# Performance work log

Measured on AMD Instinct MI355X. Metric: run time of the kernel, lower is better.

Reference implementation:

```python
import jax, jax.numpy as jnp
import numpy as np

N = 50000
E = 800000


def _degrees(src, dst):
    ones = jnp.ones((E,), dtype=jnp.float32)
    indeg = jax.ops.segment_sum(ones, dst, num_segments=N)
    outdeg = jax.ops.segment_sum(ones, src, num_segments=N)
    return indeg, outdeg


def _aggregate(h, src, dst):
    # update_all(copy_src, sum): gather src features, scatter-add to dst
    return jax.ops.segment_sum(h[src], dst, num_segments=N)


def _graph_conv(h, src, dst, innorm, outnorm, W, b):
    h = h * outnorm[:, None]
    h = _aggregate(h, src, dst)
    h = h * innorm[:, None]
    return h @ W + b


def setup_inputs() -> dict:
    key = jax.random.key(0)
    ks = jax.random.split(key, 8)
    d_in, d_hid, d_out = 128, 128, 64
    inp = {
        "features": jax.random.normal(ks[0], (N, d_in), dtype=jnp.float32),
        "src": jax.random.randint(ks[1], (E,), 0, N, dtype=jnp.int32),
        "dst": jax.random.randint(ks[2], (E,), 0, N, dtype=jnp.int32),
        "W0": jax.random.normal(ks[3], (d_in, d_hid), dtype=jnp.float32) / np.sqrt(d_in),
        "b0": jnp.zeros((d_hid,), dtype=jnp.float32),
        "W1": jax.random.normal(ks[4], (d_hid, d_hid), dtype=jnp.float32) / np.sqrt(d_hid),
        "b1": jnp.zeros((d_hid,), dtype=jnp.float32),
        "W2": jax.random.normal(ks[5], (d_hid, d_hid), dtype=jnp.float32) / np.sqrt(d_hid),
        "b2": jnp.zeros((d_hid,), dtype=jnp.float32),
        "W3": jax.random.normal(ks[6], (d_hid, d_out), dtype=jnp.float32) / np.sqrt(d_hid),
        "b3": jnp.zeros((d_out,), dtype=jnp.float32),
    }
    return inp


def reference(features, src, dst, W0, b0, W1, b1, W2, b2, W3, b3):
    indeg, outdeg = _degrees(src, dst)
    innorm = jnp.power(jnp.clip(indeg, 1.0, None), -0.5)
    outnorm = jnp.power(jnp.clip(outdeg, 1.0, None), -0.5)

    # input GraphConv + relu
    h = jax.nn.relu(_graph_conv(features, src, dst, innorm, outnorm, W0, b0))

    # GResConv blocks: graph_res=True, raw_res=True, dropout=0 (identity)
    for (W, b) in ((W1, b1), (W2, b2)):
        res = features * innorm[:, None]          # pre-norm (in-degree)
        res = _aggregate(res, src, dst)
        res = res * innorm[:, None]               # post-norm (in-degree)
        h = jax.nn.relu(_graph_conv(h, src, dst, innorm, outnorm, W, b) + res)

    # output GraphConv (no activation)
    return _graph_conv(h, src, dst, innorm, outnorm, W3, b3)
```

## Files before the change

kernel.cpp:

```cpp
#include <hip/hip_runtime.h>


#define GN 50000
#define GE 800000
#define SCAN_CHUNK 1024
#define DEG_BLOCKS 64
#define DEG_SLICE 12500
#define HALF_NODES 25000
#define HALF_WORDS 12500

__device__ __forceinline__ float u2f(unsigned int u) { return __uint_as_float(u); }

__device__ __forceinline__ unsigned int bfpack(float a, float b) {
  unsigned int ua = __float_as_uint(a); ua = (ua + 0x7fffu + ((ua >> 16) & 1u)) >> 16;
  unsigned int ub = __float_as_uint(b); ub = (ub + 0x7fffu + ((ub >> 16) & 1u)) >> 16;
  return ua | (ub << 16);
}

__device__ __forceinline__ void bfunpack8(uint4 u, float* f) {
  f[0] = u2f(u.x << 16); f[1] = u2f(u.x & 0xffff0000u);
  f[2] = u2f(u.y << 16); f[3] = u2f(u.y & 0xffff0000u);
  f[4] = u2f(u.z << 16); f[5] = u2f(u.z & 0xffff0000u);
  f[6] = u2f(u.w << 16); f[7] = u2f(u.w & 0xffff0000u);
}

__global__ __launch_bounds__(256) void degrees_lds_kernel(
    const int* __restrict__ src, const int* __restrict__ dst,
    unsigned int* __restrict__ partials, int E) {
  __shared__ unsigned int hist[HALF_WORDS];
  for (int i = threadIdx.x; i < HALF_WORDS; i += 256) hist[i] = 0u;
  __syncthreads();
  int b    = blockIdx.x & 63;
  int half = (blockIdx.x >> 6) & 1;
  int dir  = blockIdx.x >> 7;
  const int* __restrict__ idx = dir ? src : dst;
  int lo = half * HALF_NODES, hi = lo + HALF_NODES;
  int s = b * DEG_SLICE;
  int e = min(s + DEG_SLICE, E);
  for (int i = s + threadIdx.x; i < e; i += 256) {
    int node = idx[i];
    if (node >= lo && node < hi) {
      int local = node - lo;
      atomicAdd(&hist[local >> 1], 1u << ((local & 1) << 4));
    }
  }
  __syncthreads();
  unsigned int* outp = partials + (((size_t)dir * 2 + half) * DEG_BLOCKS + b) * HALF_WORDS;
  for (int i = threadIdx.x; i < HALF_WORDS; i += 256) outp[i] = hist[i];
}

__global__ void degrees_reduce_kernel(const unsigned int* __restrict__ partials,
                                      int* __restrict__ indeg, float* __restrict__ innorm,
                                      float* __restrict__ outnorm,
                                      unsigned int* __restrict__ rel16pk) {
  int g = blockIdx.x * blockDim.x + threadIdx.x;
  if (g >= 2 * HALF_WORDS) return;
  int half = (g >= HALF_WORDS) ? 1 : 0;
  int w = g - half * HALF_WORDS;
  int n0 = half * HALF_NODES + 2 * w;
  unsigned int inLo = 0, inHi = 0, outLo = 0, outHi = 0;
  const unsigned int* pIn  = partials + ((size_t)(0 * 2 + half) * DEG_BLOCKS) * HALF_WORDS + w;
  const unsigned int* pOut = partials + ((size_t)(1 * 2 + half) * DEG_BLOCKS) * HALF_WORDS + w;
#pragma unroll 4
  for (int b = 0; b < DEG_BLOCKS; b++) {
    rel16pk[((size_t)b * GN + n0) >> 1] = inLo | (inHi << 16);
    unsigned int v = pIn[(size_t)b * HALF_WORDS];
    inLo += v & 0xffffu; inHi += v >> 16;
    unsigned int u = pOut[(size_t)b * HALF_WORDS];
    outLo += u & 0xffffu; outHi += u >> 16;
  }
  indeg[n0]     = (int)inLo;
  indeg[n0 + 1] = (int)inHi;
  innorm[n0]      = rsqrtf((float)max((int)inLo, 1));
  innorm[n0 + 1]  = rsqrtf((float)max((int)inHi, 1));
  outnorm[n0]     = rsqrtf((float)max((int)outLo, 1));
  outnorm[n0 + 1] = rsqrtf((float)max((int)outHi, 1));
}

__global__ __launch_bounds__(256) void scan_blocksums(const int* __restrict__ deg,
                                                      int* __restrict__ bsums, int n) {
  int tid = threadIdx.x;
  int i = blockIdx.x * SCAN_CHUNK + tid * 4;
  int s = 0;
  if (i + 3 < n) {
    int4 v = *(const int4*)(deg + i);
    s = v.x + v.y + v.z + v.w;
  } else {
    for (int j = 0; j < 4; j++) if (i + j < n) s += deg[i + j];
  }
  for (int off = 32; off; off >>= 1) s += __shfl_down(s, off);
  __shared__ int ws[4];
  if ((tid & 63) == 0) ws[tid >> 6] = s;
  __syncthreads();
  if (tid == 0) bsums[blockIdx.x] = ws[0] + ws[1] + ws[2] + ws[3];
}

__global__ void scan_bsums(const int* __restrict__ bsums, int* __restrict__ bpref,
                           int nb, int* __restrict__ offsets, int n) {
  int tid = threadIdx.x;
  int v = (tid < nb) ? bsums[tid] : 0;
  int incl = v;
  for (int off = 1; off < 64; off <<= 1) {
    int t = __shfl_up(incl, off);
    if (tid >= off) incl += t;
  }
  if (tid < nb) bpref[tid] = incl - v;
  if (tid == 63) offsets[n] = incl;
}

__global__ __launch_bounds__(256) void scan_final(const int* __restrict__ deg,
                                                  const int* __restrict__ bpref,
                                                  int* __restrict__ offsets, int n) {
  int tid = threadIdx.x;
  int i = blockIdx.x * SCAN_CHUNK + tid * 4;
  int v[4];
#pragma unroll
  for (int j = 0; j < 4; j++) v[j] = (i + j < n) ? deg[i + j] : 0;
  int tsum = v[0] + v[1] + v[2] + v[3];
  int incl = tsum;
  for (int off = 1; off < 64; off <<= 1) {
    int t = __shfl_up(incl, off);
    if ((tid & 63) >= off) incl += t;
  }
  __shared__ int wsum[4];
  int wid = tid >> 6, lane = tid & 63;
  if (lane == 63) wsum[wid] = incl;
  __syncthreads();
  int wpref = 0;
  for (int w = 0; w < wid; w++) wpref += wsum[w];
  int run = bpref[blockIdx.x] + wpref + incl - tsum;
#pragma unroll
  for (int j = 0; j < 4; j++) {
    if (i + j < n) offsets[i + j] = run;
    run += v[j];
  }
}

__global__ __launch_bounds__(256) void fill_csr_lds_kernel(
    const int* __restrict__ src, const int* __restrict__ dst,
    const int* __restrict__ offsets, const unsigned short* __restrict__ rel16,
    int* __restrict__ csr, int E) {
  __shared__ unsigned int cnt[HALF_WORDS];
  for (int i = threadIdx.x; i < HALF_WORDS; i += 256) cnt[i] = 0u;
  __syncthreads();
  int b    = blockIdx.x & 63;
  int half = blockIdx.x >> 6;
  int lo = half * HALF_NODES, hi = lo + HALF_NODES;
  int s = b * DEG_SLICE;
  int e = min(s + DEG_SLICE, E);
  const unsigned short* relb = rel16 + (size_t)b * GN;
  for (int i = s + threadIdx.x; i < e; i += 256) {
    int d = dst[i];
    if (d >= lo && d < hi) {
      int local = d - lo;
      int sh = (local & 1) << 4;
      unsigned int old = atomicAdd(&cnt[local >> 1], 1u << sh);
      int rank = (int)((old >> sh) & 0xffffu);
      int pos = offsets[d] + (int)relb[d] + rank;
      csr[pos] = src[i];
    }
  }
}

__global__ __launch_bounds__(256) void f32_to_bf16_kernel(const float* __restrict__ in,
                                                          uint4* __restrict__ out, int n8) {
  int t = blockIdx.x * blockDim.x + threadIdx.x;
  if (t >= n8) return;
  const float4* in4 = (const float4*)in;
  float4 f0 = in4[2 * t], f1 = in4[2 * t + 1];
  uint4 o;
  o.x = bfpack(f0.x, f0.y); o.y = bfpack(f0.z, f0.w);
  o.z = bfpack(f1.x, f1.y); o.w = bfpack(f1.z, f1.w);
  out[t] = o;
}

__global__ __launch_bounds__(256) void aggregate128_bf16_kernel(
    const uint4* __restrict__ hq, const float* __restrict__ gscale,
    const float* __restrict__ wscale, const int* __restrict__ offsets,
    const int* __restrict__ csr, float* __restrict__ out, int n) {
  int node = blockIdx.x * 4 + (threadIdx.x >> 6);
  if (node >= n) return;
  int lane = threadIdx.x & 63;
  int c = lane & 15;
  int p = lane >> 4;
  int s = offsets[node], e = offsets[node + 1];
  float acc[8];
#pragma unroll
  for (int j = 0; j < 8; j++) acc[j] = 0.f;
  int i = s + p;
  for (; i + 4 < e; i += 8) {
    int sn0 = csr[i], sn1 = csr[i + 4];
    uint4 u0 = hq[(size_t)sn0 * 16 + c];
    uint4 u1 = hq[(size_t)sn1 * 16 + c];
    float s0 = gscale[sn0], s1 = gscale[sn1];
    float f0[8], f1[8];
    bfunpack8(u0, f0); bfunpack8(u1, f1);
#pragma unroll
    for (int j = 0; j < 8; j++) acc[j] += f0[j] * s0 + f1[j] * s1;
  }
  if (i < e) {
    int sn = csr[i];
    uint4 u = hq[(size_t)sn * 16 + c];
    float sc = gscale[sn];
    float f[8];
    bfunpack8(u, f);
#pragma unroll
    for (int j = 0; j < 8; j++) acc[j] += f[j] * sc;
  }
#pragma unroll
  for (int off = 32; off >= 16; off >>= 1)
#pragma unroll
    for (int j = 0; j < 8; j++) acc[j] += __shfl_down(acc[j], off);
  if (lane < 16) {
    float w = wscale[node];
    float4* orow = (float4*)(out + (size_t)node * 128);
    orow[2 * c]     = make_float4(acc[0] * w, acc[1] * w, acc[2] * w, acc[3] * w);
    orow[2 * c + 1] = make_float4(acc[4] * w, acc[5] * w, acc[6] * w, acc[7] * w);
  }
}

__global__ __launch_bounds__(256) void aggregate_dual_bf16_kernel(
    const uint4* __restrict__ hq, const float* __restrict__ g1,
    const float* __restrict__ g2, const float* __restrict__ wscale,
    const int* __restrict__ offsets, const int* __restrict__ csr,
    float* __restrict__ out1, float* __restrict__ out2, int n) {
  int node = blockIdx.x * 4 + (threadIdx.x >> 6);
  if (node >= n) return;
  int lane = threadIdx.x & 63;
  int c = lane & 15;
  int p = lane >> 4;
  int s = offsets[node], e = offsets[node + 1];
  float a1[8], a2[8];
#pragma unroll
  for (int j = 0; j < 8; j++) { a1[j] = 0.f; a2[j] = 0.f; }
  int i = s + p;
  for (; i + 4 < e; i += 8) {
    int sn0 = csr[i], sn1 = csr[i + 4];
    uint4 u0 = hq[(size_t)sn0 * 16 + c];
    uint4 u1 = hq[(size_t)sn1 * 16 + c];
    float g1a = g1[sn0], g2a = g2[sn0];
    float g1b = g1[sn1], g2b = g2[sn1];
    float f0[8], f1[8];
    bfunpack8(u0, f0); bfunpack8(u1, f1);
#pragma unroll
    for (int j = 0; j < 8; j++) {
      a1[j] += f0[j] * g1a + f1[j] * g1b;
      a2[j] += f0[j] * g2a + f1[j] * g2b;
    }
  }
  if (i < e) {
    int sn = csr[i];
    uint4 u = hq[(size_t)sn * 16 + c];
    float g1a = g1[sn], g2a = g2[sn];
    float f[8];
    bfunpack8(u, f);
#pragma unroll
    for (int j = 0; j < 8; j++) { a1[j] += f[j] * g1a; a2[j] += f[j] * g2a; }
  }
#pragma unroll
  for (int off = 32; off >= 16; off >>= 1)
#pragma unroll
    for (int j = 0; j < 8; j++) {
      a1[j] += __shfl_down(a1[j], off);
      a2[j] += __shfl_down(a2[j], off);
    }
  if (lane < 16) {
    float w = wscale[node];
    float4* o1 = (float4*)(out1 + (size_t)node * 128);
    float4* o2 = (float4*)(out2 + (size_t)node * 128);
    o1[2 * c]     = make_float4(a1[0] * w, a1[1] * w, a1[2] * w, a1[3] * w);
    o1[2 * c + 1] = make_float4(a1[4] * w, a1[5] * w, a1[6] * w, a1[7] * w);
    o2[2 * c]     = make_float4(a2[0] * w, a2[1] * w, a2[2] * w, a2[3] * w);
    o2[2 * c + 1] = make_float4(a2[4] * w, a2[5] * w, a2[6] * w, a2[7] * w);
  }
}

__global__ __launch_bounds__(256) void aggregate64_bf16_kernel(
    const uint4* __restrict__ hq, const float* __restrict__ gscale,
    const float* __restrict__ wscale, const float* __restrict__ bias,
    const int* __restrict__ offsets, const int* __restrict__ csr,
    float* __restrict__ out, int n) {
  int node = blockIdx.x * 4 + (threadIdx.x >> 6);
  if (node >= n) return;
  int lane = threadIdx.x & 63;
  int c = lane & 7;
  int p = lane >> 3;
  int s = offsets[node], e = offsets[node + 1];
  float acc[8];
#pragma unroll
  for (int j = 0; j < 8; j++) acc[j] = 0.f;
  int i = s + p;
  for (; i + 8 < e; i += 16) {
    int sn0 = csr[i], sn1 = csr[i + 8];
    uint4 u0 = hq[(size_t)sn0 * 8 + c];
    uint4 u1 = hq[(size_t)sn1 * 8 + c];
    float s0 = gscale[sn0], s1 = gscale[sn1];
    float f0[8], f1[8];
    bfunpack8(u0, f0); bfunpack8(u1, f1);
#pragma unroll
    for (int j = 0; j < 8; j++) acc[j] += f0[j] * s0 + f1[j] * s1;
  }
  if (i < e) {
    int sn = csr[i];
    uint4 u = hq[(size_t)sn * 8 + c];
    float sc = gscale[sn];
    float f[8];
    bfunpack8(u, f);
#pragma unroll
    for (int j = 0; j < 8; j++) acc[j] += f[j] * sc;
  }
#pragma unroll
  for (int off = 32; off >= 8; off >>= 1)
#pragma unroll
    for (int j = 0; j < 8; j++) acc[j] += __shfl_down(acc[j], off);
  if (lane < 8) {
    float w = wscale[node];
    const float4* bp = (const float4*)bias;
    float4 b0 = bp[2 * c], b1 = bp[2 * c + 1];
    float4* orow = (float4*)(out + (size_t)node * 64);
    orow[2 * c]     = make_float4(acc[0] * w + b0.x, acc[1] * w + b0.y,
                                  acc[2] * w + b0.z, acc[3] * w + b0.w);
    orow[2 * c + 1] = make_float4(acc[4] * w + b1.x, acc[5] * w + b1.y,
                                  acc[6] * w + b1.z, acc[7] * w + b1.w);
  }
}

template <int DOUT, bool RELU, bool HAS_BIAS, bool ADD_RES, bool OUT_BF16>
__global__ __launch_bounds__(256) void gemm_kernel(
    const float* __restrict__ A, const float* __restrict__ W,
    const float* __restrict__ bias, const float* __restrict__ res,
    void* __restrict__ outv, int n) {
  __shared__ float Wl[128 * DOUT];
  __shared__ float Al[32 * 128];
  for (int i = threadIdx.x; i < 128 * DOUT / 4; i += 256)
    ((float4*)Wl)[i] = ((const float4*)W)[i];
  int row0 = blockIdx.x * 32;
  for (int i = threadIdx.x; i < 32 * 32; i += 256) {
    int r = i >> 5, cc = i & 31;
    int gr = row0 + r;
    float4 v = make_float4(0.f, 0.f, 0.f, 0.f);
    if (gr < n) v = *((const float4*)(A + (size_t)gr * 128) + cc);
    *((float4*)(Al + r * 128) + cc) = v;
  }
  __syncthreads();
  constexpr int CG = DOUT / 4;
  constexpr int RG = 256 / CG;
  constexpr int RPT = 32 / RG;
  int tc = threadIdx.x % CG;
  int tr = threadIdx.x / CG;
  float4 acc[RPT];
#pragma unroll
  for (int r = 0; r < RPT; r++) acc[r] = make_float4(0.f, 0.f, 0.f, 0.f);
  for (int k0 = 0; k0 < 128; k0 += 4) {
    float4 av[RPT];
#pragma unroll
    for (int r = 0; r < RPT; r++)
      av[r] = *((const float4*)(Al + (tr * RPT + r) * 128 + k0));
#pragma unroll
    for (int kk = 0; kk < 4; kk++) {
      float4 w = *((const float4*)(Wl + (k0 + kk) * DOUT) + tc);
#pragma unroll
      for (int r = 0; r < RPT; r++) {
        float a = (&av[r].x)[kk];
        acc[r].x += a * w.x; acc[r].y += a * w.y;
        acc[r].z += a * w.z; acc[r].w += a * w.w;
      }
    }
  }
  float4 b = make_float4(0.f, 0.f, 0.f, 0.f);
  if (HAS_BIAS) b = ((const float4*)bias)[tc];
#pragma unroll
  for (int r = 0; r < RPT; r++) {
    int gr = row0 + tr * RPT + r;
    if (gr < n) {
      float4 o = acc[r];
      o.x += b.x; o.y += b.y; o.z += b.z; o.w += b.w;
      if (ADD_RES) {
        float4 rr = *((const float4*)(res + (size_t)gr * DOUT) + tc);
        o.x += rr.x; o.y += rr.y; o.z += rr.z; o.w += rr.w;
      }
      if (RELU) {
        o.x = fmaxf(o.x, 0.f); o.y = fmaxf(o.y, 0.f);
        o.z = fmaxf(o.z, 0.f); o.w = fmaxf(o.w, 0.f);
      }
      if (OUT_BF16) {
        uint2 pk;
        pk.x = bfpack(o.x, o.y); pk.y = bfpack(o.z, o.w);
        unsigned int* up = (unsigned int*)outv;
        *(uint2*)(up + (size_t)gr * (DOUT / 2) + tc * 2) = pk;
      } else {
        float* outp = (float*)outv;
        *((float4*)(outp + (size_t)gr * DOUT) + tc) = o;
      }
    }
  }
}

extern "C" void kernel_launch(void* const* d_in, const int* in_sizes, int n_in,
                              void* d_out, int out_size, void* d_ws, size_t ws_size,
                              hipStream_t stream) {
  const float* features = (const float*)d_in[0];
  const int*   src      = (const int*)d_in[1];
  const int*   dst      = (const int*)d_in[2];
  const float* W0 = (const float*)d_in[3];
  const float* b0 = (const float*)d_in[4];
  const float* W1 = (const float*)d_in[5];
  const float* b1 = (const float*)d_in[6];
  const float* W2 = (const float*)d_in[7];
  const float* b2 = (const float*)d_in[8];
  const float* W3 = (const float*)d_in[9];
  const float* b3 = (const float*)d_in[10];
  float* out = (float*)d_out;
  const int N = GN, E = GE;

  char* ws = (char*)d_ws;
  size_t off = 0;
  auto alloc = [&](size_t bytes) -> void* {
    void* p = ws + off;
    off = (off + bytes + 255) & ~(size_t)255;
    return p;
  };
  unsigned int* partials = (unsigned int*)alloc((size_t)2 * 2 * DEG_BLOCKS * HALF_WORDS * 4);
  unsigned int* rel16pk  = (unsigned int*)alloc((size_t)DEG_BLOCKS * GN * 2);
  int*   indeg   = (int*)alloc((size_t)N * 4);
  float* innorm  = (float*)alloc((size_t)N * 4);
  float* outnorm = (float*)alloc((size_t)N * 4);
  int*   offsets = (int*)alloc((size_t)(N + 1) * 4);
  int*   csr     = (int*)alloc((size_t)E * 4);
  int*   bsums   = (int*)alloc((size_t)256 * 4);
  int*   bpref   = (int*)alloc((size_t)256 * 4);
  float* res     = (float*)alloc((size_t)N * 128 * 4);
  float* bufA    = (float*)alloc((size_t)N * 128 * 4);
  float* bufB    = (float*)alloc((size_t)N * 128 * 4);
  uint4* hbf     = (uint4*)alloc((size_t)N * 128 * 2);
  (void)ws_size; (void)in_sizes; (void)n_in; (void)out_size;

  uint4* fbf = (uint4*)bufB;
  uint4* Ybf = (uint4*)res;

  degrees_lds_kernel<<<256, 256, 0, stream>>>(src, dst, partials, E);
  degrees_reduce_kernel<<<(2 * HALF_WORDS + 255) / 256, 256, 0, stream>>>(
      partials, indeg, innorm, outnorm, rel16pk);

  int nb = (N + SCAN_CHUNK - 1) / SCAN_CHUNK;
  scan_blocksums<<<nb, 256, 0, stream>>>(indeg, bsums, N);
  scan_bsums<<<1, 64, 0, stream>>>(bsums, bpref, nb, offsets, N);
  scan_final<<<nb, 256, 0, stream>>>(indeg, bpref, offsets, N);

  fill_csr_lds_kernel<<<128, 256, 0, stream>>>(
      src, dst, offsets, (const unsigned short*)rel16pk, csr, E);

  f32_to_bf16_kernel<<<(N * 128 / 8 + 255) / 256, 256, 0, stream>>>(
      features, fbf, N * 128 / 8);

  int aggGrid  = (N + 3) / 4;
  int gemmGrid = (N + 31) / 32;

  aggregate_dual_bf16_kernel<<<aggGrid, 256, 0, stream>>>(
      fbf, outnorm, innorm, innorm, offsets, csr, bufA, res, N);
  gemm_kernel<128, true, true, false, true><<<gemmGrid, 256, 0, stream>>>(
      bufA, W0, b0, nullptr, hbf, N);
  aggregate128_bf16_kernel<<<aggGrid, 256, 0, stream>>>(
      hbf, outnorm, innorm, offsets, csr, bufA, N);
  gemm_kernel<128, true, true, true, true><<<gemmGrid, 256, 0, stream>>>(
      bufA, W1, b1, res, hbf, N);
  aggregate128_bf16_kernel<<<aggGrid, 256, 0, stream>>>(
      hbf, outnorm, innorm, offsets, csr, bufA, N);
  gemm_kernel<128, true, true, true, false><<<gemmGrid, 256, 0, stream>>>(
      bufA, W2, b2, res, bufB, N);
  gemm_kernel<64, false, false, false, true><<<gemmGrid, 256, 0, stream>>>(
      bufB, W3, nullptr, nullptr, Ybf, N);
  aggregate64_bf16_kernel<<<aggGrid, 256, 0, stream>>>(
      Ybf, outnorm, innorm, b3, offsets, csr, out, N);
}
```

Before: 428.5 us.

## Replace FP32 LDS GEMMs with bf16 MFMA GEMMs using split-precision weights

Replaces the scalar FP32 shared-memory GEMM with an MFMA 16x16x32 bf16 kernel. Weights are pre-split into high and low bf16 parts so the weight side keeps near-FP32 accuracy, and activations are fed as bf16. The aggregation kernels now write bf16 outputs directly, which halves their write traffic and the GEMM read traffic. In exchange the activations lose precision before each matmul, and the GEMM epilogue does scalar 2-byte stores with uncoalesced residual reads.

```diff
diff --git a/kernel.cpp b/kernel.cpp
--- a/kernel.cpp
+++ b/kernel.cpp
@@ -9,14 +9,18 @@
 #define HALF_NODES 25000
 #define HALF_WORDS 12500
 
+typedef __attribute__((ext_vector_type(8))) short bf16x8;
+typedef __attribute__((ext_vector_type(4))) float f32x4;
+
 __device__ __forceinline__ float u2f(unsigned int u) { return __uint_as_float(u); }
 
+__device__ __forceinline__ unsigned int bfr(float a) {
+  unsigned int u = __float_as_uint(a);
+  return (u + 0x7fffu + ((u >> 16) & 1u)) >> 16;
+}
 __device__ __forceinline__ unsigned int bfpack(float a, float b) {
-  unsigned int ua = __float_as_uint(a); ua = (ua + 0x7fffu + ((ua >> 16) & 1u)) >> 16;
-  unsigned int ub = __float_as_uint(b); ub = (ub + 0x7fffu + ((ub >> 16) & 1u)) >> 16;
-  return ua | (ub << 16);
-}
-
+  return bfr(a) | (bfr(b) << 16);
+}
 __device__ __forceinline__ void bfunpack8(uint4 u, float* f) {
   f[0] = u2f(u.x << 16); f[1] = u2f(u.x & 0xffff0000u);
   f[2] = u2f(u.y << 16); f[3] = u2f(u.y & 0xffff0000u);
@@ -174,10 +178,31 @@
   out[t] = o;
 }
 
+__global__ __launch_bounds__(256) void wconvert_kernel(
+    const float* __restrict__ W0, const float* __restrict__ W1,
+    const float* __restrict__ W2, const float* __restrict__ W3,
+    unsigned short* __restrict__ wt) {
+  int e = blockIdx.x * 256 + threadIdx.x;
+  if (e >= 3 * 16384 + 8192) return;
+  int m, local, N;
+  if (e < 49152) { m = e >> 14; local = e & 16383; N = 128; }
+  else { m = 3; local = e - 49152; N = 64; }
+  const float* W = (m == 0) ? W0 : (m == 1) ? W1 : (m == 2) ? W2 : W3;
+  int k = local / N, n = local % N;
+  float v = W[k * N + n];
+  unsigned int hi = bfr(v);
+  float rem = v - u2f(hi << 16);
+  unsigned int lo = bfr(rem);
+  size_t hibase = (m < 3) ? (size_t)m * 32768 : 98304;
+  size_t lobase = hibase + ((m < 3) ? 16384 : 8192);
+  wt[hibase + (size_t)n * 128 + k] = (unsigned short)hi;
+  wt[lobase + (size_t)n * 128 + k] = (unsigned short)lo;
+}
+
 __global__ __launch_bounds__(256) void aggregate128_bf16_kernel(
     const uint4* __restrict__ hq, const float* __restrict__ gscale,
     const float* __restrict__ wscale, const int* __restrict__ offsets,
-    const int* __restrict__ csr, float* __restrict__ out, int n) {
+    const int* __restrict__ csr, uint4* __restrict__ outq, int n) {
   int node = blockIdx.x * 4 + (threadIdx.x >> 6);
   if (node >= n) return;
   int lane = threadIdx.x & 63;
@@ -213,9 +238,10 @@
     for (int j = 0; j < 8; j++) acc[j] += __shfl_down(acc[j], off);
   if (lane < 16) {
     float w = wscale[node];
-    float4* orow = (float4*)(out + (size_t)node * 128);
-    orow[2 * c]     = make_float4(acc[0] * w, acc[1] * w, acc[2] * w, acc[3] * w);
-    orow[2 * c + 1] = make_float4(acc[4] * w, acc[5] * w, acc[6] * w, acc[7] * w);
+    uint4 q;
+    q.x = bfpack(acc[0] * w, acc[1] * w); q.y = bfpack(acc[2] * w, acc[3] * w);
+    q.z = bfpack(acc[4] * w, acc[5] * w); q.w = bfpack(acc[6] * w, acc[7] * w);
+    outq[(size_t)node * 16 + c] = q;
   }
 }
 
@@ -223,7 +249,7 @@
     const uint4* __restrict__ hq, const float* __restrict__ g1,
     const float* __restrict__ g2, const float* __restrict__ wscale,
     const int* __restrict__ offsets, const int* __restrict__ csr,
-    float* __restrict__ out1, float* __restrict__ out2, int n) {
+    uint4* __restrict__ out1q, float* __restrict__ out2, int n) {
   int node = blockIdx.x * 4 + (threadIdx.x >> 6);
   if (node >= n) return;
   int lane = threadIdx.x & 63;
@@ -266,10 +292,11 @@
     }
   if (lane < 16) {
     float w = wscale[node];
-    float4* o1 = (float4*)(out1 + (size_t)node * 128);
+    uint4 q;
+    q.x = bfpack(a1[0] * w, a1[1] * w); q.y = bfpack(a1[2] * w, a1[3] * w);
+    q.z = bfpack(a1[4] * w, a1[5] * w); q.w = bfpack(a1[6] * w, a1[7] * w);
+    out1q[(size_t)node * 16 + c] = q;
     float4* o2 = (float4*)(out2 + (size_t)node * 128);
-    o1[2 * c]     = make_float4(a1[0] * w, a1[1] * w, a1[2] * w, a1[3] * w);
-    o1[2 * c + 1] = make_float4(a1[4] * w, a1[5] * w, a1[6] * w, a1[7] * w);
     o2[2 * c]     = make_float4(a2[0] * w, a2[1] * w, a2[2] * w, a2[3] * w);
     o2[2 * c + 1] = make_float4(a2[4] * w, a2[5] * w, a2[6] * w, a2[7] * w);
   }
@@ -325,72 +352,61 @@
   }
 }
 
-template <int DOUT, bool RELU, bool HAS_BIAS, bool ADD_RES, bool OUT_BF16>
-__global__ __launch_bounds__(256) void gemm_kernel(
-    const float* __restrict__ A, const float* __restrict__ W,
-    const float* __restrict__ bias, const float* __restrict__ res,
-    void* __restrict__ outv, int n) {
-  __shared__ float Wl[128 * DOUT];
-  __shared__ float Al[32 * 128];
-  for (int i = threadIdx.x; i < 128 * DOUT / 4; i += 256)
-    ((float4*)Wl)[i] = ((const float4*)W)[i];
-  int row0 = blockIdx.x * 32;
-  for (int i = threadIdx.x; i < 32 * 32; i += 256) {
-    int r = i >> 5, cc = i & 31;
-    int gr = row0 + r;
-    float4 v = make_float4(0.f, 0.f, 0.f, 0.f);
-    if (gr < n) v = *((const float4*)(A + (size_t)gr * 128) + cc);
-    *((float4*)(Al + r * 128) + cc) = v;
-  }
-  __syncthreads();
-  constexpr int CG = DOUT / 4;
-  constexpr int RG = 256 / CG;
-  constexpr int RPT = 32 / RG;
-  int tc = threadIdx.x % CG;
-  int tr = threadIdx.x / CG;
-  float4 acc[RPT];
-#pragma unroll
-  for (int r = 0; r < RPT; r++) acc[r] = make_float4(0.f, 0.f, 0.f, 0.f);
-  for (int k0 = 0; k0 < 128; k0 += 4) {
-    float4 av[RPT];
-#pragma unroll
-    for (int r = 0; r < RPT; r++)
-      av[r] = *((const float4*)(Al + (tr * RPT + r) * 128 + k0));
-#pragma unroll
-    for (int kk = 0; kk < 4; kk++) {
-      float4 w = *((const float4*)(Wl + (k0 + kk) * DOUT) + tc);
-#pragma unroll
-      for (int r = 0; r < RPT; r++) {
-        float a = (&av[r].x)[kk];
-        acc[r].x += a * w.x; acc[r].y += a * w.y;
-        acc[r].z += a * w.z; acc[r].w += a * w.w;
-      }
-    }
-  }
-  float4 b = make_float4(0.f, 0.f, 0.f, 0.f);
-  if (HAS_BIAS) b = ((const float4*)bias)[tc];
-#pragma unroll
-  for (int r = 0; r < RPT; r++) {
-    int gr = row0 + tr * RPT + r;
-    if (gr < n) {
-      float4 o = acc[r];
-      o.x += b.x; o.y += b.y; o.z += b.z; o.w += b.w;
-      if (ADD_RES) {
-        float4 rr = *((const float4*)(res + (size_t)gr * DOUT) + tc);
-        o.x += rr.x; o.y += rr.y; o.z += rr.z; o.w += rr.w;
-      }
-      if (RELU) {
-        o.x = fmaxf(o.x, 0.f); o.y = fmaxf(o.y, 0.f);
-        o.z = fmaxf(o.z, 0.f); o.w = fmaxf(o.w, 0.f);
-      }
-      if (OUT_BF16) {
-        uint2 pk;
-        pk.x = bfpack(o.x, o.y); pk.y = bfpack(o.z, o.w);
-        unsigned int* up = (unsigned int*)outv;
-        *(uint2*)(up + (size_t)gr * (DOUT / 2) + tc * 2) = pk;
-      } else {
-        float* outp = (float*)outv;
-        *((float4*)(outp + (size_t)gr * DOUT) + tc) = o;
+template <int NT, bool RELU, bool HAS_BIAS, bool ADD_RES>
+__global__ __launch_bounds__(256) void mfma_gemm_kernel(
+    const unsigned short* __restrict__ Abf, const unsigned short* __restrict__ Wth,
+    const unsigned short* __restrict__ Wtl, const float* __restrict__ bias,
+    const float* __restrict__ res, unsigned short* __restrict__ outbf, int M) {
+  constexpr int DOUT = NT * 16;
+  int wid = threadIdx.x >> 6, lane = threadIdx.x & 63;
+  int row0 = (blockIdx.x * 4 + wid) * 32;
+  int lr = lane & 15, g = lane >> 4;
+  bf16x8 a[2][4];
+  bf16x8 zz = {0, 0, 0, 0, 0, 0, 0, 0};
+#pragma unroll
+  for (int rt = 0; rt < 2; rt++) {
+    int r = row0 + rt * 16 + lr;
+    if (r < M) {
+      const unsigned short* ap = Abf + (size_t)r * 128 + g * 8;
+#pragma unroll
+      for (int s = 0; s < 4; s++) a[rt][s] = *(const bf16x8*)(ap + s * 32);
+    } else {
+#pragma unroll
+      for (int s = 0; s < 4; s++) a[rt][s] = zz;
+    }
+  }
+#pragma unroll
+  for (int ct = 0; ct < NT; ct++) {
+    const unsigned short* wph = Wth + (size_t)(ct * 16 + lr) * 128 + g * 8;
+    const unsigned short* wpl = Wtl + (size_t)(ct * 16 + lr) * 128 + g * 8;
+    bf16x8 wh[4], wl[4];
+#pragma unroll
+    for (int s = 0; s < 4; s++) {
+      wh[s] = *(const bf16x8*)(wph + s * 32);
+      wl[s] = *(const bf16x8*)(wpl + s * 32);
+    }
+    f32x4 acc0 = {0.f, 0.f, 0.f, 0.f}, acc1 = {0.f, 0.f, 0.f, 0.f};
+#pragma unroll
+    for (int s = 0; s < 4; s++) {
+      acc0 = __builtin_amdgcn_mfma_f32_16x16x32_bf16(a[0][s], wh[s], acc0, 0, 0, 0);
+      acc0 = __builtin_amdgcn_mfma_f32_16x16x32_bf16(a[0][s], wl[s], acc0, 0, 0, 0);
+      acc1 = __builtin_amdgcn_mfma_f32_16x16x32_bf16(a[1][s], wh[s], acc1, 0, 0, 0);
+      acc1 = __builtin_amdgcn_mfma_f32_16x16x32_bf16(a[1][s], wl[s], acc1, 0, 0, 0);
+    }
+    int col = ct * 16 + lr;
+    float bv = HAS_BIAS ? bias[col] : 0.f;
+#pragma unroll
+    for (int rt = 0; rt < 2; rt++) {
+      f32x4 acc = rt ? acc1 : acc0;
+#pragma unroll
+      for (int j = 0; j < 4; j++) {
+        int r = row0 + rt * 16 + g * 4 + j;
+        if (r < M) {
+          float v = acc[j] + bv;
+          if (ADD_RES) v += res[(size_t)r * 128 + col];
+          if (RELU) v = fmaxf(v, 0.f);
+          outbf[(size_t)r * DOUT + col] = (unsigned short)bfr(v);
+        }
       }
     }
   }
@@ -429,14 +445,18 @@
   int*   csr     = (int*)alloc((size_t)E * 4);
   int*   bsums   = (int*)alloc((size_t)256 * 4);
   int*   bpref   = (int*)alloc((size_t)256 * 4);
-  float* res     = (float*)alloc((size_t)N * 128 * 4);
-  float* bufA    = (float*)alloc((size_t)N * 128 * 4);
-  float* bufB    = (float*)alloc((size_t)N * 128 * 4);
-  uint4* hbf     = (uint4*)alloc((size_t)N * 128 * 2);
+  unsigned short* wt = (unsigned short*)alloc((size_t)114688 * 2);
+  uint4* fbf = (uint4*)alloc((size_t)N * 128 * 2);
+  float* res = (float*)alloc((size_t)N * 128 * 4);
+  unsigned short* tbf = (unsigned short*)alloc((size_t)N * 128 * 2);
+  unsigned short* hbf = (unsigned short*)alloc((size_t)N * 128 * 2);
   (void)ws_size; (void)in_sizes; (void)n_in; (void)out_size;
 
-  uint4* fbf = (uint4*)bufB;
-  uint4* Ybf = (uint4*)res;
+  unsigned short* Ybf = (unsigned short*)res;
+  const unsigned short *w0h = wt,          *w0l = wt + 16384;
+  const unsigned short *w1h = wt + 32768,  *w1l = wt + 49152;
+  const unsigned short *w2h = wt + 65536,  *w2l = wt + 81920;
+  const unsigned short *w3h = wt + 98304,  *w3l = wt + 106496;
 
   degrees_lds_kernel<<<256, 256, 0, stream>>>(src, dst, partials, E);
   degrees_reduce_kernel<<<(2 * HALF_WORDS + 255) / 256, 256, 0, stream>>>(
@@ -450,26 +470,27 @@
   fill_csr_lds_kernel<<<128, 256, 0, stream>>>(
       src, dst, offsets, (const unsigned short*)rel16pk, csr, E);
 
+  wconvert_kernel<<<(57344 + 255) / 256, 256, 0, stream>>>(W0, W1, W2, W3, wt);
   f32_to_bf16_kernel<<<(N * 128 / 8 + 255) / 256, 256, 0, stream>>>(
       features, fbf, N * 128 / 8);
 
   int aggGrid  = (N + 3) / 4;
-  int gemmGrid = (N + 31) / 32;
+  int gemmGrid = (N + 127) / 128;
 
   aggregate_dual_bf16_kernel<<<aggGrid, 256, 0, stream>>>(
-      fbf, outnorm, innorm, innorm, offsets, csr, bufA, res, N);
-  gemm_kernel<128, true, true, false, true><<<gemmGrid, 256, 0, stream>>>(
-      bufA, W0, b0, nullptr, hbf, N);
+      fbf, outnorm, innorm, innorm, offsets, csr, (uint4*)tbf, res, N);
+  mfma_gemm_kernel<8, true, true, false><<<gemmGrid, 256, 0, stream>>>(
+      tbf, w0h, w0l, b0, nullptr, hbf, N);
   aggregate128_bf16_kernel<<<aggGrid, 256, 0, stream>>>(
-      hbf, outnorm, innorm, offsets, csr, bufA, N);
-  gemm_kernel<128, true, true, true, true><<<gemmGrid, 256, 0, stream>>>(
-      bufA, W1, b1, res, hbf, N);
+      (const uint4*)hbf, outnorm, innorm, offsets, csr, (uint4*)tbf, N);
+  mfma_gemm_kernel<8, true, true, true><<<gemmGrid, 256, 0, stream>>>(
+      tbf, w1h, w1l, b1, res, hbf, N);
   aggregate128_bf16_kernel<<<aggGrid, 256, 0, stream>>>(
-      hbf, outnorm, innorm, offsets, csr, bufA, N);
-  gemm_kernel<128, true, true, true, false><<<gemmGrid, 256, 0, stream>>>(
-      bufA, W2, b2, res, bufB, N);
-  gemm_kernel<64, false, false, false, true><<<gemmGrid, 256, 0, stream>>>(
-      bufB, W3, nullptr, nullptr, Ybf, N);
+      (const uint4*)hbf, outnorm, innorm, offsets, csr, (uint4*)tbf, N);
+  mfma_gemm_kernel<8, true, true, true><<<gemmGrid, 256, 0, stream>>>(
+      tbf, w2h, w2l, b2, res, hbf, N);
+  mfma_gemm_kernel<4, false, false, false><<<gemmGrid, 256, 0, stream>>>(
+      hbf, w3h, w3l, nullptr, nullptr, Ybf, N);
   aggregate64_bf16_kernel<<<aggGrid, 256, 0, stream>>>(
-      Ybf, outnorm, innorm, b3, offsets, csr, out, N);
-}
+      (const uint4*)Ybf, outnorm, innorm, b3, offsets, csr, out, N);
+}
```

Result: faster. 385.3 us (-10.1%).
